# Optimization experiments

Hardware: AMD Instinct MI355X
Metric: run time of the kernel (lower is better)

## Reference

```python
import jax, jax.numpy as jnp
import numpy as np
from jax import lax

DEPTH = 2
HEADS = 8
TEMP = 1.0

def _ln_last(x, g, b, eps=1e-5):
    m = x.mean(-1, keepdims=True)
    v = ((x - m) ** 2).mean(-1, keepdims=True)
    return (x - m) / jnp.sqrt(v + eps) * g + b

def _ln_chan(x, g, b, eps=1e-6):
    # torch custom LayerNorm over channel dim of NCHW, biased var
    m = x.mean(1, keepdims=True)
    v = ((x - m) ** 2).mean(1, keepdims=True)
    return (x - m) / jnp.sqrt(v + eps) * g[None, :, None, None] + b[None, :, None, None]

def _conv3x3(x, w):
    return lax.conv_general_dilated(x, w, (1, 1), ((1, 1), (1, 1)),
                                    dimension_numbers=('NCHW', 'OIHW', 'NCHW'))

def _transformer(x, ln1_g, ln1_b, qkv_w, qkv_b, out_w, out_b, ln2_g, ln2_b,
                 mlp_w1, mlp_b1, mlp_w2, mlp_b2):
    dim = x.shape[-1]
    dh = dim // HEADS
    scale = dh ** -0.5
    for i in range(DEPTH):
        h = _ln_last(x, ln1_g[i], ln1_b[i])
        qkv = h @ qkv_w[i] + qkv_b[i]
        q, k, v = jnp.split(qkv, 3, axis=-1)
        sp = lambda t: t.reshape(t.shape[0], t.shape[1], HEADS, dh).transpose(0, 2, 1, 3)
        q, k, v = sp(q), sp(k), sp(v)
        attn = jax.nn.softmax(jnp.einsum('bhid,bhjd->bhij', q, k) * scale, axis=-1) / TEMP
        o = jnp.einsum('bhij,bhjd->bhid', attn, v).transpose(0, 2, 1, 3).reshape(x.shape)
        x = o @ out_w[i] + out_b[i] + x
        h = _ln_last(x, ln2_g[i], ln2_b[i])
        x = jax.nn.gelu(h @ mlp_w1[i] + mlp_b1[i], approximate=False) @ mlp_w2[i] + mlp_b2[i] + x
    return x

def _tacf(support_feature, query_feature, task_descriptor, ln1_g, ln1_b, qkv_w, qkv_b,
          out_w, out_b, ln2_g, ln2_b, mlp_w1, mlp_b1, mlp_w2, mlp_b2,
          rfm_ln_g, rfm_ln_b, rfm_conv1, rfm_conv2, rfm_conv3, rfm_conv4):
    n, c, h, w = support_feature.shape
    M = task_descriptor.shape[1]
    # descriptor generator: 'n c h w -> 1 (n h w) c', prepend descriptors
    sf = support_feature.transpose(0, 2, 3, 1).reshape(1, n * h * w, c)
    x = jnp.concatenate([task_descriptor, sf], axis=1)
    x = _transformer(x, ln1_g, ln1_b, qkv_w, qkv_b, out_w, out_b, ln2_g, ln2_b,
                     mlp_w1, mlp_b1, mlp_w2, mlp_b2)
    key0 = x[0, :M, :]  # (M, C)

    def region(feat):
        # mean over C of feat[:,None,c,h,w]*key[m,c] == matmul / C
        return jax.nn.sigmoid(jnp.einsum('bchw,mc->bmhw', feat, key0) / feat.shape[1])

    def map_fuse(reg, feat):
        # mean over m of (feat*task + feat) == feat*(mean_m(task)+1)
        return feat * (reg.mean(1, keepdims=True) + 1.0)

    def rfm(x4):
        t = _ln_chan(x4, rfm_ln_g, rfm_ln_b)
        t = jax.nn.relu(_conv3x3(t, rfm_conv1))
        t = jax.nn.relu(_conv3x3(t, rfm_conv2))
        t = jax.nn.relu(_conv3x3(t, rfm_conv3))
        t = _conv3x3(t, rfm_conv4)
        b_, T_, h_, w_ = t.shape
        t = jax.nn.sigmoid(t.reshape(b_, T_, h_ * w_))  # (B,T,HW)
        feat = x4.transpose(0, 2, 3, 1).reshape(b_, h_ * w_, -1)  # (B,HW,C)
        out = jnp.einsum('btp,bpc->btc', t, feat) / (h_ * w_)  # mean over HW
        return out.transpose(0, 2, 1)  # (B,C,T)

    qr = region(query_feature)
    sr = region(support_feature)
    aq = map_fuse(qr, query_feature)
    asp = map_fuse(sr, support_feature)
    return (rfm(asp), rfm(aq))

def setup_inputs() -> dict:
    key = jax.random.key(0)
    ks = jax.random.split(key, 12)
    B_S, B_Q, C, H, W = 25, 75, 128, 10, 10
    M, T, MLP = 16, 32, 512
    rn = lambda k, s, sc=1.0: jax.random.normal(k, s, dtype=jnp.float32) * sc
    return {
        'support_feature': rn(ks[0], (B_S, C, H, W)),
        'query_feature': rn(ks[1], (B_Q, C, H, W)),
        'task_descriptor': rn(ks[2], (1, M, C)),
        'ln1_g': jnp.ones((DEPTH, C), jnp.float32), 'ln1_b': jnp.zeros((DEPTH, C), jnp.float32),
        'qkv_w': rn(ks[3], (DEPTH, C, 3 * C), 0.02), 'qkv_b': jnp.zeros((DEPTH, 3 * C), jnp.float32),
        'out_w': rn(ks[4], (DEPTH, C, C), 0.02), 'out_b': jnp.zeros((DEPTH, C), jnp.float32),
        'ln2_g': jnp.ones((DEPTH, C), jnp.float32), 'ln2_b': jnp.zeros((DEPTH, C), jnp.float32),
        'mlp_w1': rn(ks[5], (DEPTH, C, MLP), 0.02), 'mlp_b1': jnp.zeros((DEPTH, MLP), jnp.float32),
        'mlp_w2': rn(ks[6], (DEPTH, MLP, C), 0.02), 'mlp_b2': jnp.zeros((DEPTH, C), jnp.float32),
        'rfm_ln_g': jnp.ones((C,), jnp.float32), 'rfm_ln_b': jnp.zeros((C,), jnp.float32),
        'rfm_conv1': rn(ks[7], (T, C, 3, 3), 0.05),
        'rfm_conv2': rn(ks[8], (T, T, 3, 3), 0.05),
        'rfm_conv3': rn(ks[9], (T, T, 3, 3), 0.05),
        'rfm_conv4': rn(ks[10], (T, T, 3, 3), 0.05),
    }

def reference(support_feature, query_feature, task_descriptor, ln1_g, ln1_b, qkv_w, qkv_b,
              out_w, out_b, ln2_g, ln2_b, mlp_w1, mlp_b1, mlp_w2, mlp_b2,
              rfm_ln_g, rfm_ln_b, rfm_conv1, rfm_conv2, rfm_conv3, rfm_conv4):
    return _tacf(support_feature, query_feature, task_descriptor, ln1_g, ln1_b, qkv_w, qkv_b,
                 out_w, out_b, ln2_g, ln2_b, mlp_w1, mlp_b1, mlp_w2, mlp_b2,
                 rfm_ln_g, rfm_ln_b, rfm_conv1, rfm_conv2, rfm_conv3, rfm_conv4)
```

## Files before the change

kernel.cpp:

```cpp
#include <hip/hip_runtime.h>
#include <math.h>

#define SEQ 2516
#define SEQP 2520
#define SEQP2 2560
#define CDIM 128

typedef __attribute__((ext_vector_type(8))) short short8;
typedef __attribute__((ext_vector_type(4))) float f32x4;

__device__ __forceinline__ float gelu_exact(float x) {
    return x * 0.5f * (1.0f + erff(x * 0.7071067811865475f));
}
__device__ __forceinline__ float fexp2(float x) { return __builtin_amdgcn_exp2f(x); }
__device__ __forceinline__ short f2bf(float f) {
    unsigned u = __float_as_uint(f);
    unsigned r = 0x7fffu + ((u >> 16) & 1u);
    return (short)((u + r) >> 16);
}
__device__ __forceinline__ short f2bf_trunc(float f) {
    return (short)(__float_as_uint(f) >> 16);
}

__global__ __launch_bounds__(64) void concat_ln_kernel(
// ... 71 lines not shown
    #pragma unroll
    for (int ns = 0; ns < 4; ++ns) {
        const int n = n0 + ns * 16 + c16;
        float bv = bias[n];
        #pragma unroll
        for (int r = 0; r < 4; ++r) {
            const int row = m0 + wave * 16 + quad * 4 + r;
            float v = acc[ns][r] + bv;
            if (region == 0)      Qbf[(size_t)row * 128 + n] = f2bf(v * SC);
            else if (region == 1) Kbf[(size_t)row * 128 + (n - 128)] = f2bf(v);
            else                  VTb[(size_t)(n - 256) * SEQP2 + row] = f2bf(v);
        }
    }
}

__global__ __launch_bounds__(256) void mlp_fused_kernel(
    const float* __restrict__ A, const float* __restrict__ W1,
    const float* __restrict__ b1, const float* __restrict__ W2,
    float* __restrict__ PARTG) {
    __shared__ __align__(16) short W1t[64 * 136];
    __shared__ __align__(16) short W2t[128 * 72];
    __shared__ __align__(16) short Ct[4 * 16 * 72];
    const int t = threadIdx.x;
    const int wave = t >> 6, lane = t & 63;
    const int quad = lane >> 4, c16 = lane & 15;
    const int m0 = blockIdx.x * 64;
    const int kz = blockIdx.y;
    const int n0 = kz * 64;
    #pragma unroll
    for (int pass = 0; pass < 4; ++pass) {
        int idx = t + pass * 256;
        int n = idx & 63, kc = idx >> 6;
        short8 wv;
        #pragma unroll
        for (int j = 0; j < 8; ++j)
            wv[j] = f2bf(W1[(size_t)(kc * 8 + j) * 512 + n0 + n]);
        *(short8*)&W1t[n * 136 + kc * 8] = wv;
    }
    {
        const int n = t & 127, half = t >> 7;
        #pragma unroll
        for (int c = 0; c < 4; ++c) {
            short8 wv;
            #pragma unroll
            for (int j = 0; j < 8; ++j)
                wv[j] = f2bf(W2[(size_t)(n0 + half * 32 + c * 8 + j) * 128 + n]);
            *(short8*)&W2t[n * 72 + half * 32 + c * 8] = wv;
        }
    }
    __syncthreads();
    const int am = m0 + wave * 16 + c16;
    f32x4 acc1[4];
    #pragma unroll
    for (int i = 0; i < 4; ++i) acc1[i] = (f32x4){0.f, 0.f, 0.f, 0.f};
    #pragma unroll
    for (int kk = 0; kk < 4; ++kk) {
        const float4* ap = (const float4*)(A + (size_t)am * 128 + kk * 32 + quad * 8);
        float4 a0 = ap[0], a1 = ap[1];
        short8 af;
        af[0] = f2bf(a0.x); af[1] = f2bf(a0.y); af[2] = f2bf(a0.z); af[3] = f2bf(a0.w);
        af[4] = f2bf(a1.x); af[5] = f2bf(a1.y); af[6] = f2bf(a1.z); af[7] = f2bf(a1.w);
        #pragma unroll
        for (int ns = 0; ns < 4; ++ns) {
            short8 wf = *(const short8*)&W1t[(ns * 16 + c16) * 136 + kk * 32 + quad * 8];
            acc1[ns] = __builtin_amdgcn_mfma_f32_16x16x32_bf16(af, wf, acc1[ns], 0, 0, 0);
        }
    }
    short* Cw = Ct + wave * 16 * 72;
    #pragma unroll
    for (int ns = 0; ns < 4; ++ns) {
        float bv = b1[n0 + ns * 16 + c16];
        #pragma unroll
        for (int r = 0; r < 4; ++r)
            Cw[(quad * 4 + r) * 72 + ns * 16 + c16] = f2bf(gelu_exact(acc1[ns][r] + bv));
    }
    f32x4 acc2[8];
    #pragma unroll
    for (int i = 0; i < 8; ++i) acc2[i] = (f32x4){0.f, 0.f, 0.f, 0.f};
    #pragma unroll
    for (int kk = 0; kk < 2; ++kk) {
        short8 af2 = *(const short8*)&Cw[c16 * 72 + kk * 32 + quad * 8];
        #pragma unroll
        for (int ns = 0; ns < 8; ++ns) {
            short8 wf = *(const short8*)&W2t[(ns * 16 + c16) * 72 + kk * 32 + quad * 8];
            acc2[ns] = __builtin_amdgcn_mfma_f32_16x16x32_bf16(af2, wf, acc2[ns], 0, 0, 0);
        }
    }
    float* dst = PARTG + (size_t)kz * SEQP2 * 128;
    #pragma unroll
    for (int ns = 0; ns < 8; ++ns) {
        #pragma unroll
        for (int r = 0; r < 4; ++r) {
            const int row = m0 + wave * 16 + quad * 4 + r;
            dst[(size_t)row * 128 + ns * 16 + c16] = acc2[ns][r];
        }
    }
}

__global__ __launch_bounds__(512) void combine_ln_kernel(
    const float* __restrict__ PARTG, const float* __restrict__ bias,
    const float* __restrict__ R, float* __restrict__ C, float* __restrict__ H,
    const float* __restrict__ g, const float* __restrict__ bb, int M) {
    __shared__ float ln[8][130];
    const int t = threadIdx.x;
    const int c = t & 127;
    const int grp = __builtin_amdgcn_readfirstlane(t >> 7);
    const int r0 = blockIdx.x * 8 + grp * 2;
    #pragma unroll
    for (int i = 0; i < 2; ++i) {
        const int row = r0 + i;
        float v = bias[c] + R[(size_t)row * 128 + c];
        #pragma unroll
        for (int kz = 0; kz < 8; ++kz)
            v += PARTG[(size_t)kz * SEQP2 * 128 + (size_t)row * 128 + c];
        ln[grp * 2 + i][c] = v;
        if (row < M) C[(size_t)row * 128 + c] = v;
    }
    __syncthreads();
    const int wv = t >> 6, l = t & 63;
    float x0 = ln[wv][l], x1 = ln[wv][l + 64];
    float s = x0 + x1;
    for (int off = 32; off > 0; off >>= 1) s += __shfl_down(s, off);
    float mean = __shfl(s, 0) * (1.f / 128.f);
    float d0 = x0 - mean, d1 = x1 - mean;
    float vv = d0 * d0 + d1 * d1;
    for (int off = 32; off > 0; off >>= 1) vv += __shfl_down(vv, off);
    float var = __shfl(vv, 0) * (1.f / 128.f);
    float rstd = rsqrtf(var + 1e-5f);
    const int hrow = blockIdx.x * 8 + wv;
    H[(size_t)hrow * 128 + l]      = d0 * rstd * g[l] + bb[l];
    H[(size_t)hrow * 128 + 64 + l] = d1 * rstd * g[l + 64] + bb[l + 64];
}

__global__ __launch_bounds__(512) void proj_merge_ln_kernel(
    const float* __restrict__ PART, const float* __restrict__ W,
    const float* __restrict__ bias, const float* __restrict__ R,
    float* __restrict__ C, float* __restrict__ H,
    const float* __restrict__ g, const float* __restrict__ bb, int M) {
    __shared__ float ln[8][130];
    const int t = threadIdx.x;
    const int c = t & 127;
    const int grp = __builtin_amdgcn_readfirstlane(t >> 7);
    const int r0 = blockIdx.x * 8 + grp * 2;
    float acc0 = 0.f, acc1 = 0.f;
    #pragma unroll
    for (int h = 0; h < 8; ++h) {
        const float* p0a = PART + ((size_t)h * SEQP + r0) * 20;
        const float* p1a = PART + ((size_t)(8 + h) * SEQP + r0) * 20;
        const float* p0b = p0a + 20;
        const float* p1b = p1a + 20;
        float m0 = p0a[16], l0 = p0a[17], m1 = p1a[16], l1 = p1a[17];
        float Ma = fmaxf(m0, m1);
        float w0 = fexp2(m0 - Ma), w1 = fexp2(m1 - Ma);
        float inva = 1.f / fmaf(l0, w0, l1 * w1);
        float c0a = w0 * inva, c1a = w1 * inva;
        m0 = p0b[16]; l0 = p0b[17]; m1 = p1b[16]; l1 = p1b[17];
        float Mb = fmaxf(m0, m1);
        w0 = fexp2(m0 - Mb); w1 = fexp2(m1 - Mb);
        float invb = 1.f / fmaf(l0, w0, l1 * w1);
        float c0b = w0 * invb, c1b = w1 * invb;
        #pragma unroll
        for (int kk = 0; kk < 4; ++kk) {
            const int k0 = h * 16 + kk * 4;
            float w_0 = W[(size_t)(k0 + 0) * 128 + c];
            float w_1 = W[(size_t)(k0 + 1) * 128 + c];
            float w_2 = W[(size_t)(k0 + 2) * 128 + c];
            float w_3 = W[(size_t)(k0 + 3) * 128 + c];
            float4 x0 = *(const float4*)&p0a[kk * 4];
            float4 y0 = *(const float4*)&p1a[kk * 4];
            float4 x1 = *(const float4*)&p0b[kk * 4];
            float4 y1 = *(const float4*)&p1b[kk * 4];
            float a00 = x0.x * c0a + y0.x * c1a;
            float a01 = x0.y * c0a + y0.y * c1a;
            float a02 = x0.z * c0a + y0.z * c1a;
            float a03 = x0.w * c0a + y0.w * c1a;
            float a10 = x1.x * c0b + y1.x * c1b;
            float a11 = x1.y * c0b + y1.y * c1b;
            float a12 = x1.z * c0b + y1.z * c1b;
            float a13 = x1.w * c0b + y1.w * c1b;
            acc0 = fmaf(a00, w_0, acc0); acc0 = fmaf(a01, w_1, acc0);
            acc0 = fmaf(a02, w_2, acc0); acc0 = fmaf(a03, w_3, acc0);
            acc1 = fmaf(a10, w_0, acc1); acc1 = fmaf(a11, w_1, acc1);
            acc1 = fmaf(a12, w_2, acc1); acc1 = fmaf(a13, w_3, acc1);
        }
    }
    float bv = bias[c];
    float v0 = acc0 + bv + R[(size_t)(r0 + 0) * 128 + c];
    float v1 = acc1 + bv + R[(size_t)(r0 + 1) * 128 + c];
    ln[grp * 2 + 0][c] = v0;
    ln[grp * 2 + 1][c] = v1;
    if (r0 + 0 < M) C[(size_t)(r0 + 0) * 128 + c] = v0;
    if (r0 + 1 < M) C[(size_t)(r0 + 1) * 128 + c] = v1;
    __syncthreads();
    const int wv = t >> 6, l = t & 63;
    float x0 = ln[wv][l], x1 = ln[wv][l + 64];
    float s = x0 + x1;
    for (int off = 32; off > 0; off >>= 1) s += __shfl_down(s, off);
    float mean = __shfl(s, 0) * (1.f / 128.f);
    float d0 = x0 - mean, d1 = x1 - mean;
    float vv = d0 * d0 + d1 * d1;
    for (int off = 32; off > 0; off >>= 1) vv += __shfl_down(vv, off);
    float var = __shfl(vv, 0) * (1.f / 128.f);
    float rstd = rsqrtf(var + 1e-5f);
    const int hrow = blockIdx.x * 8 + wv;
    H[(size_t)hrow * 128 + l]      = d0 * rstd * g[l] + bb[l];
    H[(size_t)hrow * 128 + 64 + l] = d1 * rstd * g[l + 64] + bb[l + 64];
}

__global__ __launch_bounds__(128) void attn_kernel(
    const short* __restrict__ Qbf, const short* __restrict__ Kbf,
    const short* __restrict__ VTb, float* __restrict__ PART) {
    __shared__ __align__(16) short sKs[9600];
    short* Ks = sKs;
    short* Vt = sKs + 3072;
    const int t = threadIdx.x;
    const int wave = t >> 6, lane = t & 63;
    const int quad = lane >> 4, c16 = lane & 15;
    short* Pw = sKs + 3072 + 2176 + wave * 16 * 136;
    const int head = blockIdx.y, z = blockIdx.z;
    const int qb = blockIdx.x * 32 + wave * 16;

    short8 qf;
    #pragma unroll
// ... 75 lines not shown
    for (int r = 0; r < 4; ++r) {
        float lr = l_[r];
        lr += __shfl_xor(lr, 1);
        lr += __shfl_xor(lr, 2);
        lr += __shfl_xor(lr, 4);
        lr += __shfl_xor(lr, 8);
        const int qrow = qb + quad * 4 + r;
        if (qrow < SEQ) {
            float* dst = PART + ((size_t)(z * 8 + head) * SEQP + qrow) * 20;
            dst[c16] = oacc[r];
            if (c16 == 0) { dst[16] = m_[r]; dst[17] = lr; }
        }
    }
}

__global__ __launch_bounds__(256) void region_fuse_stats_kernel(
    const float* __restrict__ sup, const float* __restrict__ qry,
    const float* __restrict__ X, float* __restrict__ fused,
    float* __restrict__ MEAN, float* __restrict__ RSTD) {
    __shared__ float key0[2048];
    __shared__ float rfac[100];
    const int b = blockIdx.x;
    const int t = threadIdx.x;
    const float* feat = (b < 25) ? (sup + (size_t)b * 12800) : (qry + (size_t)(b - 25) * 12800);
    for (int i = t; i < 2048; i += 256) key0[i] = X[i];
    __syncthreads();
    if (t < 100) {
        float dots[16];
        #pragma unroll
        for (int mm = 0; mm < 16; ++mm) dots[mm] = 0.f;
        float s = 0.f, ss = 0.f;
        for (int c = 0; c < 128; ++c) {
            float f = feat[c * 100 + t];
            s += f; ss += f * f;
            #pragma unroll
            for (int mm = 0; mm < 16; ++mm) dots[mm] += f * key0[mm * 128 + c];
        }
        float mean16 = 0.f;
        #pragma unroll
        for (int mm = 0; mm < 16; ++mm) mean16 += 1.f / (1.f + expf(-dots[mm] * (1.f / 128.f)));
        float r = mean16 * (1.f / 16.f) + 1.f;
        rfac[t] = r;
        float mr = s * (1.f / 128.f);
        float vr = ss * (1.f / 128.f) - mr * mr;
        MEAN[b * 128 + t] = mr * r;
        RSTD[b * 128 + t] = rsqrtf(vr * r * r + 1e-6f);
    }
    __syncthreads();
    for (int i = t; i < 12800; i += 256)
        fused[(size_t)b * 12800 + i] = feat[i] * rfac[i % 100];
}

__global__ __launch_bounds__(256) void conv1_split_kernel(
    const float* __restrict__ in, const float* __restrict__ w,
    const float* __restrict__ MEAN, const float* __restrict__ RSTD,
    const float* __restrict__ g, const float* __restrict__ bb,
    float* __restrict__ PARTC) {
    __shared__ float sin_[32 * 144];
    const int b = blockIdx.x;
    const int base_to = blockIdx.y * 8;
    const int cb = blockIdx.z * 32;
    const int t = threadIdx.x;
    const int h = __builtin_amdgcn_readfirstlane(t >> 7);
    const int p = t & 127;
    const int py = p / 10, px = p - py * 10;
    const bool active = p < 100;
    float acc[4] = {0.f, 0.f, 0.f, 0.f};
    for (int i = t; i < 32 * 144; i += 256) {
        int c = i / 144, pos = i - c * 144;
        int y = pos / 12 - 1, x = pos % 12 - 1;
        float v = 0.f;
        if ((unsigned)y < 10u && (unsigned)x < 10u) {
            int pp = y * 10 + x;
            float raw = in[(size_t)b * 12800 + (cb + c) * 100 + pp];
            v = (raw - MEAN[b * 128 + pp]) * RSTD[b * 128 + pp] * g[cb + c] + bb[cb + c];
        }
        sin_[i] = v;
    }
    __syncthreads();
    if (active) {
        const float* wbase = w + ((size_t)(base_to + h * 4) * 128 + cb) * 9;
        for (int c = 0; c < 32; ++c) {
            const float* sp = &sin_[c * 144 + py * 12 + px];
            float pix[9];
            #pragma unroll
            for (int k = 0; k < 9; ++k) pix[k] = sp[(k / 3) * 12 + (k % 3)];
            #pragma unroll
            for (int j = 0; j < 4; ++j) {
                const float* wq = wbase + ((size_t)j * 128 + c) * 9;
                #pragma unroll
                for (int k = 0; k < 9; ++k) acc[j] = fmaf(pix[k], wq[k], acc[j]);
            }
        }
        #pragma unroll
        for (int j = 0; j < 4; ++j)
            PARTC[((size_t)blockIdx.z * 100 + b) * 3200 + (base_to + h * 4 + j) * 100 + p] = acc[j];
    }
}

template<bool RELU, bool COMBINE>
__global__ __launch_bounds__(256) void conv3x3_to4_kernel(
    const float* __restrict__ in, const float* __restrict__ w,
    float* __restrict__ out) {
    __shared__ float sin_[32 * 144];
    const int b = blockIdx.x;
    const int base_to = blockIdx.y * 4;
    const int t = threadIdx.x;
    const int h = __builtin_amdgcn_readfirstlane(t >> 7);
    const int p = t & 127;
    const int py = p / 10, px = p - py * 10;
    const bool active = p < 100;
    float acc[2] = {0.f, 0.f};
    for (int i = t; i < 32 * 144; i += 256) {
        int c = i / 144, pos = i - c * 144;
        int y = pos / 12 - 1, x = pos % 12 - 1;
        float v = 0.f;
        if ((unsigned)y < 10u && (unsigned)x < 10u) {
            if (COMBINE) {
                const size_t base = (size_t)b * 3200 + c * 100 + y * 10 + x;
                v = in[base] + in[base + 320000] + in[base + 640000] + in[base + 960000];
                v = fmaxf(v, 0.f);
            } else {
                v = in[(size_t)b * 3200 + c * 100 + y * 10 + x];
            }
        }
        sin_[i] = v;
    }
    __syncthreads();
    if (active) {
        const float* wbase = w + ((size_t)(base_to + h * 2) * 32) * 9;
        for (int c = 0; c < 32; ++c) {
            const float* sp = &sin_[c * 144 + py * 12 + px];
            float pix[9];
            #pragma unroll
            for (int k = 0; k < 9; ++k) pix[k] = sp[(k / 3) * 12 + (k % 3)];
            #pragma unroll
            for (int j = 0; j < 2; ++j) {
                const float* wq = wbase + ((size_t)j * 32 + c) * 9;
                #pragma unroll
                for (int k = 0; k < 9; ++k) acc[j] = fmaf(pix[k], wq[k], acc[j]);
            }
        }
        #pragma unroll
        for (int j = 0; j < 2; ++j) {
            float v = acc[j];
            if (RELU) v = fmaxf(v, 0.f);
            out[(size_t)b * 3200 + (base_to + h * 2 + j) * 100 + p] = v;
        }
    }
}

__global__ __launch_bounds__(256) void conv4_rfm_kernel(
    const float* __restrict__ in, const float* __restrict__ w,
    const float* __restrict__ fused, float* __restrict__ out) {
    __shared__ float sin_[32 * 144];
    __shared__ float sig[4][104];
    const int b = blockIdx.x;
    const int base_to = blockIdx.y * 4;
    const int t = threadIdx.x;
    const int h = __builtin_amdgcn_readfirstlane(t >> 7);
    const int p = t & 127;
    const int py = p / 10, px = p - py * 10;
    const bool active = p < 100;
    float acc[2] = {0.f, 0.f};
    for (int i = t; i < 32 * 144; i += 256) {
        int c = i / 144, pos = i - c * 144;
        int y = pos / 12 - 1, x = pos % 12 - 1;
        float v = 0.f;
        if ((unsigned)y < 10u && (unsigned)x < 10u)
            v = in[(size_t)b * 3200 + c * 100 + y * 10 + x];
        sin_[i] = v;
    }
    __syncthreads();
    if (active) {
        const float* wbase = w + ((size_t)(base_to + h * 2) * 32) * 9;
        for (int c = 0; c < 32; ++c) {
            const float* sp = &sin_[c * 144 + py * 12 + px];
            float pix[9];
            #pragma unroll
            for (int k = 0; k < 9; ++k) pix[k] = sp[(k / 3) * 12 + (k % 3)];
            #pragma unroll
            for (int j = 0; j < 2; ++j) {
                const float* wq = wbase + ((size_t)j * 32 + c) * 9;
                #pragma unroll
                for (int k = 0; k < 9; ++k) acc[j] = fmaf(pix[k], wq[k], acc[j]);
            }
        }
        sig[h * 2 + 0][p] = 1.f / (1.f + expf(-acc[0]));
        sig[h * 2 + 1][p] = 1.f / (1.f + expf(-acc[1]));
    }
    __syncthreads();
    #pragma unroll
    for (int rep = 0; rep < 2; ++rep) {
        const int o = t + rep * 256;
        const int cc = o >> 2, ttl = o & 3;
        const float* fp = fused + (size_t)b * 12800 + cc * 100;
        float s = 0.f;
        for (int pp = 0; pp < 100; pp += 4) {
            float4 f4 = *(const float4*)&fp[pp];
            s += sig[ttl][pp] * f4.x + sig[ttl][pp + 1] * f4.y
               + sig[ttl][pp + 2] * f4.z + sig[ttl][pp + 3] * f4.w;
        }
        out[(size_t)b * 4096 + cc * 32 + base_to + ttl] = s * 0.01f;
    }
}

extern "C" void kernel_launch(void* const* d_in, const int* in_sizes, int n_in,
                              void* d_out, int out_size, void* d_ws, size_t ws_size,
                              hipStream_t stream) {
    (void)in_sizes; (void)n_in; (void)out_size; (void)ws_size;
    const float* sup    = (const float*)d_in[0];
    const float* qry    = (const float*)d_in[1];
    const float* td     = (const float*)d_in[2];
    const float* ln1_g  = (const float*)d_in[3];
    const float* ln1_b  = (const float*)d_in[4];
    const float* qkv_w  = (const float*)d_in[5];
    const float* qkv_b  = (const float*)d_in[6];
    const float* out_w  = (const float*)d_in[7];
// ... 3 lines not shown
    const float* mlp_w1 = (const float*)d_in[11];
    const float* mlp_b1 = (const float*)d_in[12];
    const float* mlp_w2 = (const float*)d_in[13];
    const float* mlp_b2 = (const float*)d_in[14];
    const float* rg     = (const float*)d_in[15];
    const float* rb     = (const float*)d_in[16];
    const float* c1     = (const float*)d_in[17];
    const float* c2     = (const float*)d_in[18];
    const float* c3     = (const float*)d_in[19];
    const float* c4     = (const float*)d_in[20];
    float* out = (float*)d_out;

    float* ws   = (float*)d_ws;
    float* X    = ws;
    float* H    = X + 327680;
    float* PARTC= H + 327680;
    float* FUSED= PARTC + 1280000;
    float* MEAN = FUSED + 1280000;
    float* RSTD = MEAN + 12800;
    float* CB1  = RSTD + 12800;
    float* CB2  = CB1 + 320000;
    short* Qbf  = (short*)(CB2 + 320000);
    short* Kbf  = Qbf + 327680;
    short* VTb  = Kbf + 327680;
    float* PARTG= (float*)(VTb + 327680);
    float* PART = PARTG;

    const int SG = (SEQ + 7) / 8;
    const int MT = (SEQ + 63) / 64;

    concat_ln_kernel<<<SEQ, 64, 0, stream>>>(td, sup, ln1_g, ln1_b, X, H);
    for (int i = 0; i < 2; ++i) {
        const int qmt    = (i == 0) ? MT : 1;
        const int atiles = (i == 0) ? (SEQ + 31) / 32 : 1;
        const int sg     = (i == 0) ? SG : 2;
        const int mmt    = (i == 0) ? MT : 1;
        qkv_mfma_kernel<<<dim3(MT, 6), 256, 0, stream>>>(
            H, qkv_w + (size_t)i * 128 * 384, qkv_b + i * 384, Qbf, Kbf, VTb, qmt);
        attn_kernel<<<dim3(atiles, 8, 2), 128, 0, stream>>>(Qbf, Kbf, VTb, PART);
        proj_merge_ln_kernel<<<sg, 512, 0, stream>>>(
            PART, out_w + (size_t)i * 128 * 128, out_b + i * 128, X, X, H,
            ln2_g + i * 128, ln2_b + i * 128, SEQ);
        mlp_fused_kernel<<<dim3(mmt, 8), 256, 0, stream>>>(
            H, mlp_w1 + (size_t)i * 128 * 512, mlp_b1 + i * 512,
            mlp_w2 + (size_t)i * 512 * 128, PARTG);
        const float* ng = (i == 0) ? ln1_g + 128 : ln1_g;
        const float* nb = (i == 0) ? ln1_b + 128 : ln1_b;
        combine_ln_kernel<<<sg, 512, 0, stream>>>(
            PARTG, mlp_b2 + i * 128, X, X, H, ng, nb, SEQ);
    }
    region_fuse_stats_kernel<<<100, 256, 0, stream>>>(sup, qry, X, FUSED, MEAN, RSTD);
    conv1_split_kernel<<<dim3(100, 4, 4), 256, 0, stream>>>(FUSED, c1, MEAN, RSTD, rg, rb, PARTC);
    conv3x3_to4_kernel<true,  true ><<<dim3(100, 8), 256, 0, stream>>>(PARTC, c2, CB2);
    conv3x3_to4_kernel<true,  false><<<dim3(100, 8), 256, 0, stream>>>(CB2, c3, CB1);
    conv4_rfm_kernel<<<dim3(100, 8), 256, 0, stream>>>(CB1, c4, FUSED, out);
}
```

Baseline: 316.6 us.

## Fuse out-projection, LN, MLP into one kernel and collapse conv chain into megakernel

The attention merge, output projection, residual, LayerNorm, both MLP GEMMs, a second residual and the next LayerNorm now run in one MFMA kernel per 64-row tile. This removes the split-K MLP partial buffer and two extra launches per layer. The region-fuse, channel LayerNorm and four 3x3 conv stages also merge into a single 512-thread kernel per image that keeps intermediates in shared memory. In exchange, parallelism drops: 40 blocks for the MLP instead of 320, and 100 blocks for the whole conv chain instead of up to 1600. Each block also loops serially over eight MLP weight chunks.

New measurement: 500.0 us. +57.9%, slower.

```diff
diff --git a/kernel.cpp b/kernel.cpp
--- a/kernel.cpp
+++ b/kernel.cpp
@@ -109,199 +109,6 @@
     }
 }
 
-__global__ __launch_bounds__(256) void mlp_fused_kernel(
-    const float* __restrict__ A, const float* __restrict__ W1,
-    const float* __restrict__ b1, const float* __restrict__ W2,
-    float* __restrict__ PARTG) {
-    __shared__ __align__(16) short W1t[64 * 136];
-    __shared__ __align__(16) short W2t[128 * 72];
-    __shared__ __align__(16) short Ct[4 * 16 * 72];
-    const int t = threadIdx.x;
-    const int wave = t >> 6, lane = t & 63;
-    const int quad = lane >> 4, c16 = lane & 15;
-    const int m0 = blockIdx.x * 64;
-    const int kz = blockIdx.y;
-    const int n0 = kz * 64;
-    #pragma unroll
-    for (int pass = 0; pass < 4; ++pass) {
-        int idx = t + pass * 256;
-        int n = idx & 63, kc = idx >> 6;
-        short8 wv;
-        #pragma unroll
-        for (int j = 0; j < 8; ++j)
-            wv[j] = f2bf(W1[(size_t)(kc * 8 + j) * 512 + n0 + n]);
-        *(short8*)&W1t[n * 136 + kc * 8] = wv;
-    }
-    {
-        const int n = t & 127, half = t >> 7;
-        #pragma unroll
-        for (int c = 0; c < 4; ++c) {
-            short8 wv;
-            #pragma unroll
-            for (int j = 0; j < 8; ++j)
-                wv[j] = f2bf(W2[(size_t)(n0 + half * 32 + c * 8 + j) * 128 + n]);
-            *(short8*)&W2t[n * 72 + half * 32 + c * 8] = wv;
-        }
-    }
-    __syncthreads();
-    const int am = m0 + wave * 16 + c16;
-    f32x4 acc1[4];
-    #pragma unroll
-    for (int i = 0; i < 4; ++i) acc1[i] = (f32x4){0.f, 0.f, 0.f, 0.f};
-    #pragma unroll
-    for (int kk = 0; kk < 4; ++kk) {
-        const float4* ap = (const float4*)(A + (size_t)am * 128 + kk * 32 + quad * 8);
-        float4 a0 = ap[0], a1 = ap[1];
-        short8 af;
-        af[0] = f2bf(a0.x); af[1] = f2bf(a0.y); af[2] = f2bf(a0.z); af[3] = f2bf(a0.w);
-        af[4] = f2bf(a1.x); af[5] = f2bf(a1.y); af[6] = f2bf(a1.z); af[7] = f2bf(a1.w);
-        #pragma unroll
-        for (int ns = 0; ns < 4; ++ns) {
-            short8 wf = *(const short8*)&W1t[(ns * 16 + c16) * 136 + kk * 32 + quad * 8];
-            acc1[ns] = __builtin_amdgcn_mfma_f32_16x16x32_bf16(af, wf, acc1[ns], 0, 0, 0);
-        }
-    }
-    short* Cw = Ct + wave * 16 * 72;
-    #pragma unroll
-    for (int ns = 0; ns < 4; ++ns) {
-        float bv = b1[n0 + ns * 16 + c16];
-        #pragma unroll
-        for (int r = 0; r < 4; ++r)
-            Cw[(quad * 4 + r) * 72 + ns * 16 + c16] = f2bf(gelu_exact(acc1[ns][r] + bv));
-    }
-    f32x4 acc2[8];
-    #pragma unroll
-    for (int i = 0; i < 8; ++i) acc2[i] = (f32x4){0.f, 0.f, 0.f, 0.f};
-    #pragma unroll
-    for (int kk = 0; kk < 2; ++kk) {
-        short8 af2 = *(const short8*)&Cw[c16 * 72 + kk * 32 + quad * 8];
-        #pragma unroll
-        for (int ns = 0; ns < 8; ++ns) {
-            short8 wf = *(const short8*)&W2t[(ns * 16 + c16) * 72 + kk * 32 + quad * 8];
-            acc2[ns] = __builtin_amdgcn_mfma_f32_16x16x32_bf16(af2, wf, acc2[ns], 0, 0, 0);
-        }
-    }
-    float* dst = PARTG + (size_t)kz * SEQP2 * 128;
-    #pragma unroll
-    for (int ns = 0; ns < 8; ++ns) {
-        #pragma unroll
-        for (int r = 0; r < 4; ++r) {
-            const int row = m0 + wave * 16 + quad * 4 + r;
-            dst[(size_t)row * 128 + ns * 16 + c16] = acc2[ns][r];
-        }
-    }
-}
-
-__global__ __launch_bounds__(512) void combine_ln_kernel(
-    const float* __restrict__ PARTG, const float* __restrict__ bias,
-    const float* __restrict__ R, float* __restrict__ C, float* __restrict__ H,
-    const float* __restrict__ g, const float* __restrict__ bb, int M) {
-    __shared__ float ln[8][130];
-    const int t = threadIdx.x;
-    const int c = t & 127;
-    const int grp = __builtin_amdgcn_readfirstlane(t >> 7);
-    const int r0 = blockIdx.x * 8 + grp * 2;
-    #pragma unroll
-    for (int i = 0; i < 2; ++i) {
-        const int row = r0 + i;
-        float v = bias[c] + R[(size_t)row * 128 + c];
-        #pragma unroll
-        for (int kz = 0; kz < 8; ++kz)
-            v += PARTG[(size_t)kz * SEQP2 * 128 + (size_t)row * 128 + c];
-        ln[grp * 2 + i][c] = v;
-        if (row < M) C[(size_t)row * 128 + c] = v;
-    }
-    __syncthreads();
-    const int wv = t >> 6, l = t & 63;
-    float x0 = ln[wv][l], x1 = ln[wv][l + 64];
-    float s = x0 + x1;
-    for (int off = 32; off > 0; off >>= 1) s += __shfl_down(s, off);
-    float mean = __shfl(s, 0) * (1.f / 128.f);
-    float d0 = x0 - mean, d1 = x1 - mean;
-    float vv = d0 * d0 + d1 * d1;
-    for (int off = 32; off > 0; off >>= 1) vv += __shfl_down(vv, off);
-    float var = __shfl(vv, 0) * (1.f / 128.f);
-    float rstd = rsqrtf(var + 1e-5f);
-    const int hrow = blockIdx.x * 8 + wv;
-    H[(size_t)hrow * 128 + l]      = d0 * rstd * g[l] + bb[l];
-    H[(size_t)hrow * 128 + 64 + l] = d1 * rstd * g[l + 64] + bb[l + 64];
-}
-
-__global__ __launch_bounds__(512) void proj_merge_ln_kernel(
-    const float* __restrict__ PART, const float* __restrict__ W,
-    const float* __restrict__ bias, const float* __restrict__ R,
-    float* __restrict__ C, float* __restrict__ H,
-    const float* __restrict__ g, const float* __restrict__ bb, int M) {
-    __shared__ float ln[8][130];
-    const int t = threadIdx.x;
-    const int c = t & 127;
-    const int grp = __builtin_amdgcn_readfirstlane(t >> 7);
-    const int r0 = blockIdx.x * 8 + grp * 2;
-    float acc0 = 0.f, acc1 = 0.f;
-    #pragma unroll
-    for (int h = 0; h < 8; ++h) {
-        const float* p0a = PART + ((size_t)h * SEQP + r0) * 20;
-        const float* p1a = PART + ((size_t)(8 + h) * SEQP + r0) * 20;
-        const float* p0b = p0a + 20;
-        const float* p1b = p1a + 20;
-        float m0 = p0a[16], l0 = p0a[17], m1 = p1a[16], l1 = p1a[17];
-        float Ma = fmaxf(m0, m1);
-        float w0 = fexp2(m0 - Ma), w1 = fexp2(m1 - Ma);
-        float inva = 1.f / fmaf(l0, w0, l1 * w1);
-        float c0a = w0 * inva, c1a = w1 * inva;
-        m0 = p0b[16]; l0 = p0b[17]; m1 = p1b[16]; l1 = p1b[17];
-        float Mb = fmaxf(m0, m1);
-        w0 = fexp2(m0 - Mb); w1 = fexp2(m1 - Mb);
-        float invb = 1.f / fmaf(l0, w0, l1 * w1);
-        float c0b = w0 * invb, c1b = w1 * invb;
-        #pragma unroll
-        for (int kk = 0; kk < 4; ++kk) {
-            const int k0 = h * 16 + kk * 4;
-            float w_0 = W[(size_t)(k0 + 0) * 128 + c];
-            float w_1 = W[(size_t)(k0 + 1) * 128 + c];
-            float w_2 = W[(size_t)(k0 + 2) * 128 + c];
-            float w_3 = W[(size_t)(k0 + 3) * 128 + c];
-            float4 x0 = *(const float4*)&p0a[kk * 4];
-            float4 y0 = *(const float4*)&p1a[kk * 4];
-            float4 x1 = *(const float4*)&p0b[kk * 4];
-            float4 y1 = *(const float4*)&p1b[kk * 4];
-            float a00 = x0.x * c0a + y0.x * c1a;
-            float a01 = x0.y * c0a + y0.y * c1a;
-            float a02 = x0.z * c0a + y0.z * c1a;
-            float a03 = x0.w * c0a + y0.w * c1a;
-            float a10 = x1.x * c0b + y1.x * c1b;
-            float a11 = x1.y * c0b + y1.y * c1b;
-            float a12 = x1.z * c0b + y1.z * c1b;
-            float a13 = x1.w * c0b + y1.w * c1b;
-            acc0 = fmaf(a00, w_0, acc0); acc0 = fmaf(a01, w_1, acc0);
-            acc0 = fmaf(a02, w_2, acc0); acc0 = fmaf(a03, w_3, acc0);
-            acc1 = fmaf(a10, w_0, acc1); acc1 = fmaf(a11, w_1, acc1);
-            acc1 = fmaf(a12, w_2, acc1); acc1 = fmaf(a13, w_3, acc1);
-        }
-    }
-    float bv = bias[c];
-    float v0 = acc0 + bv + R[(size_t)(r0 + 0) * 128 + c];
-    float v1 = acc1 + bv + R[(size_t)(r0 + 1) * 128 + c];
-    ln[grp * 2 + 0][c] = v0;
-    ln[grp * 2 + 1][c] = v1;
-    if (r0 + 0 < M) C[(size_t)(r0 + 0) * 128 + c] = v0;
-    if (r0 + 1 < M) C[(size_t)(r0 + 1) * 128 + c] = v1;
-    __syncthreads();
-    const int wv = t >> 6, l = t & 63;
-    float x0 = ln[wv][l], x1 = ln[wv][l + 64];
-    float s = x0 + x1;
-    for (int off = 32; off > 0; off >>= 1) s += __shfl_down(s, off);
-    float mean = __shfl(s, 0) * (1.f / 128.f);
-    float d0 = x0 - mean, d1 = x1 - mean;
-    float vv = d0 * d0 + d1 * d1;
-    for (int off = 32; off > 0; off >>= 1) vv += __shfl_down(vv, off);
-    float var = __shfl(vv, 0) * (1.f / 128.f);
-    float rstd = rsqrtf(var + 1e-5f);
-    const int hrow = blockIdx.x * 8 + wv;
-    H[(size_t)hrow * 128 + l]      = d0 * rstd * g[l] + bb[l];
-    H[(size_t)hrow * 128 + 64 + l] = d1 * rstd * g[l + 64] + bb[l + 64];
-}
-
 __global__ __launch_bounds__(128) void attn_kernel(
     const short* __restrict__ Qbf, const short* __restrict__ Kbf,
     const short* __restrict__ VTb, float* __restrict__ PART) {
@@ -407,194 +214,357 @@
     }
 }
 
-__global__ __launch_bounds__(256) void region_fuse_stats_kernel(
+__global__ __launch_bounds__(256) void pml_kernel(
+    const float* __restrict__ PART, const float* __restrict__ Wo,
+    const float* __restrict__ ob, const float* __restrict__ g2,
+    const float* __restrict__ bl2, const float* __restrict__ W1,
+    const float* __restrict__ b1, const float* __restrict__ W2,
+    const float* __restrict__ b2, const float* __restrict__ gn,
+    const float* __restrict__ bn,
+    float* __restrict__ X, float* __restrict__ H) {
+    __shared__ __align__(16) short hA[64 * 136];
+    __shared__ __align__(16) short U[23040];
+    const int t = threadIdx.x;
+    const int wave = t >> 6, lane = t & 63;
+    const int quad = lane >> 4, c16 = lane & 15;
+    const int m0 = blockIdx.x * 64;
+
+    for (int i = t; i < 16384; i += 256) {
+        int n = i & 127, k = i >> 7;
+        U[n * 136 + k] = f2bf(Wo[k * 128 + n]);
+    }
+    __syncthreads();
+    const int am = m0 + wave * 16 + c16;
+    const int amc = (am < SEQ) ? am : (SEQ - 1);
+    const bool okrow = (am < SEQ);
+    f32x4 acc[8];
+    #pragma unroll
+    for (int i = 0; i < 8; ++i) acc[i] = (f32x4){0.f, 0.f, 0.f, 0.f};
+    #pragma unroll
+    for (int kk = 0; kk < 4; ++kk) {
+        const int head = kk * 2 + (quad >> 1);
+        const int d0 = (quad & 1) * 8;
+        const float* P0 = PART + ((size_t)head * SEQP + amc) * 20;
+        const float* P1 = PART + ((size_t)(8 + head) * SEQP + amc) * 20;
+        float ma = P0[16], la = P0[17], mb = P1[16], lb = P1[17];
+        float Mx = fmaxf(ma, mb);
+        float w0 = fexp2(ma - Mx), w1 = fexp2(mb - Mx);
+        float inv = 1.f / fmaf(la, w0, lb * w1);
+        float c0 = okrow ? w0 * inv : 0.f;
+        float c1 = okrow ? w1 * inv : 0.f;
+        float4 xlo = *(const float4*)&P0[d0];
+        float4 xhi = *(const float4*)&P0[d0 + 4];
+        float4 ylo = *(const float4*)&P1[d0];
+        float4 yhi = *(const float4*)&P1[d0 + 4];
+        short8 af;
+        af[0] = f2bf(xlo.x * c0 + ylo.x * c1);
+        af[1] = f2bf(xlo.y * c0 + ylo.y * c1);
+        af[2] = f2bf(xlo.z * c0 + ylo.z * c1);
+        af[3] = f2bf(xlo.w * c0 + ylo.w * c1);
+        af[4] = f2bf(xhi.x * c0 + yhi.x * c1);
+        af[5] = f2bf(xhi.y * c0 + yhi.y * c1);
+        af[6] = f2bf(xhi.z * c0 + yhi.z * c1);
+        af[7] = f2bf(xhi.w * c0 + yhi.w * c1);
+        #pragma unroll
+        for (int ns = 0; ns < 8; ++ns) {
+            short8 wf = *(const short8*)&U[(ns * 16 + c16) * 136 + kk * 32 + quad * 8];
+            acc[ns] = __builtin_amdgcn_mfma_f32_16x16x32_bf16(af, wf, acc[ns], 0, 0, 0);
+        }
+    }
+    const int row0 = m0 + wave * 16 + quad * 4;
+    f32x4 xp[8];
+    #pragma unroll
+    for (int ns = 0; ns < 8; ++ns) {
+        const int col = ns * 16 + c16;
+        float bv = ob[col];
+        #pragma unroll
+        for (int r = 0; r < 4; ++r)
+            xp[ns][r] = acc[ns][r] + bv + X[(size_t)(row0 + r) * 128 + col];
+    }
+    #pragma unroll
+    for (int r = 0; r < 4; ++r) {
+        float sm = 0.f;
+        #pragma unroll
+        for (int ns = 0; ns < 8; ++ns) sm += xp[ns][r];
+        sm += __shfl_xor(sm, 1); sm += __shfl_xor(sm, 2);
+        sm += __shfl_xor(sm, 4); sm += __shfl_xor(sm, 8);
+        float mu = sm * (1.f / 128.f);
+        float vs = 0.f;
+        #pragma unroll
+        for (int ns = 0; ns < 8; ++ns) { float d = xp[ns][r] - mu; vs = fmaf(d, d, vs); }
+        vs += __shfl_xor(vs, 1); vs += __shfl_xor(vs, 2);
+        vs += __shfl_xor(vs, 4); vs += __shfl_xor(vs, 8);
+        float rs = rsqrtf(vs * (1.f / 128.f) + 1e-5f);
+        #pragma unroll
+        for (int ns = 0; ns < 8; ++ns) {
+            const int col = ns * 16 + c16;
+            float hv = (xp[ns][r] - mu) * rs * g2[col] + bl2[col];
+            hA[(wave * 16 + quad * 4 + r) * 136 + col] = f2bf(hv);
+        }
+    }
+
+    f32x4 acc2[8];
+    #pragma unroll
+    for (int i = 0; i < 8; ++i) acc2[i] = (f32x4){0.f, 0.f, 0.f, 0.f};
+    for (int kz = 0; kz < 8; ++kz) {
+        __syncthreads();
+        #pragma unroll
+        for (int pass = 0; pass < 4; ++pass) {
+            int idx = t + pass * 256;
+            int n = idx & 63, kc = idx >> 6;
+            short8 wv;
+            #pragma unroll
+            for (int j = 0; j < 8; ++j)
+                wv[j] = f2bf(W1[(size_t)(kc * 8 + j) * 512 + kz * 64 + n]);
+            *(short8*)&U[n * 136 + kc * 8] = wv;
+        }
+        {
+            const int n = t & 127, half = t >> 7;
+            #pragma unroll
+            for (int c = 0; c < 4; ++c) {
+                short8 wv;
+                #pragma unroll
+                for (int j = 0; j < 8; ++j)
+                    wv[j] = f2bf(W2[(size_t)(kz * 64 + half * 32 + c * 8 + j) * 128 + n]);
+                *(short8*)&U[8704 + n * 72 + half * 32 + c * 8] = wv;
+            }
+        }
+        __syncthreads();
+        f32x4 acc1[4];
+        #pragma unroll
+        for (int i = 0; i < 4; ++i) acc1[i] = (f32x4){0.f, 0.f, 0.f, 0.f};
+        #pragma unroll
+        for (int kk = 0; kk < 4; ++kk) {
+            short8 af = *(const short8*)&hA[(wave * 16 + c16) * 136 + kk * 32 + quad * 8];
+            #pragma unroll
+            for (int ns = 0; ns < 4; ++ns) {
+                short8 wf = *(const short8*)&U[(ns * 16 + c16) * 136 + kk * 32 + quad * 8];
+                acc1[ns] = __builtin_amdgcn_mfma_f32_16x16x32_bf16(af, wf, acc1[ns], 0, 0, 0);
+            }
+        }
+        short* Cw = &U[17920 + wave * 16 * 72];
+        #pragma unroll
+        for (int ns = 0; ns < 4; ++ns) {
+            float bv = b1[kz * 64 + ns * 16 + c16];
+            #pragma unroll
+            for (int r = 0; r < 4; ++r)
+                Cw[(quad * 4 + r) * 72 + ns * 16 + c16] = f2bf(gelu_exact(acc1[ns][r] + bv));
+        }
+        #pragma unroll
+        for (int kk = 0; kk < 2; ++kk) {
+            short8 af2 = *(const short8*)&Cw[c16 * 72 + kk * 32 + quad * 8];
+            #pragma unroll
+            for (int ns = 0; ns < 8; ++ns) {
+                short8 wf = *(const short8*)&U[8704 + (ns * 16 + c16) * 72 + kk * 32 + quad * 8];
+                acc2[ns] = __builtin_amdgcn_mfma_f32_16x16x32_bf16(af2, wf, acc2[ns], 0, 0, 0);
+            }
+        }
+    }
+    #pragma unroll
+    for (int ns = 0; ns < 8; ++ns) {
+        const int col = ns * 16 + c16;
+        float bv = b2[col];
+        #pragma unroll
+        for (int r = 0; r < 4; ++r) {
+            float v = acc2[ns][r] + bv + xp[ns][r];
+            xp[ns][r] = v;
+            X[(size_t)(row0 + r) * 128 + col] = v;
+        }
+    }
+    #pragma unroll
+    for (int r = 0; r < 4; ++r) {
+        float sm = 0.f;
+        #pragma unroll
+        for (int ns = 0; ns < 8; ++ns) sm += xp[ns][r];
+        sm += __shfl_xor(sm, 1); sm += __shfl_xor(sm, 2);
+        sm += __shfl_xor(sm, 4); sm += __shfl_xor(sm, 8);
+        float mu = sm * (1.f / 128.f);
+        float vs = 0.f;
+        #pragma unroll
+        for (int ns = 0; ns < 8; ++ns) { float d = xp[ns][r] - mu; vs = fmaf(d, d, vs); }
+        vs += __shfl_xor(vs, 1); vs += __shfl_xor(vs, 2);
+        vs += __shfl_xor(vs, 4); vs += __shfl_xor(vs, 8);
+        float rs = rsqrtf(vs * (1.f / 128.f) + 1e-5f);
+        #pragma unroll
+        for (int ns = 0; ns < 8; ++ns) {
+            const int col = ns * 16 + c16;
+            H[(size_t)(row0 + r) * 128 + col] = (xp[ns][r] - mu) * rs * gn[col] + bn[col];
+        }
+    }
+}
+
+__global__ __launch_bounds__(512) void conv_mega_kernel(
     const float* __restrict__ sup, const float* __restrict__ qry,
-    const float* __restrict__ X, float* __restrict__ fused,
-    float* __restrict__ MEAN, float* __restrict__ RSTD) {
-    __shared__ float key0[2048];
-    __shared__ float rfac[100];
+    const float* __restrict__ X,
+    const float* __restrict__ rg, const float* __restrict__ rb,
+    const float* __restrict__ w1, const float* __restrict__ w2,
+    const float* __restrict__ w3, const float* __restrict__ w4,
+    float* __restrict__ out) {
+    __shared__ float bufA[32 * 144];
+    __shared__ float bufB[32 * 144];
+    __shared__ float sigw[32][105];
+    __shared__ float dotsL[16][100];
+    __shared__ float rfacL[100], MEANL[100], RSTDL[100];
     const int b = blockIdx.x;
     const int t = threadIdx.x;
     const float* feat = (b < 25) ? (sup + (size_t)b * 12800) : (qry + (size_t)(b - 25) * 12800);
-    for (int i = t; i < 2048; i += 256) key0[i] = X[i];
+
+    for (int task = t; task < 1600; task += 512) {
+        int m = task / 100, p = task - m * 100;
+        const float* kp = X + m * 128;
+        float d = 0.f;
+        for (int c = 0; c < 128; ++c) d = fmaf(feat[c * 100 + p], kp[c], d);
+        dotsL[m][p] = d;
+    }
+    float s = 0.f, ss = 0.f;
+    if (t < 100) {
+        for (int c = 0; c < 128; ++c) {
+            float f = feat[c * 100 + t];
+            s += f; ss = fmaf(f, f, ss);
+        }
+    }
+    for (int i = t; i < 32 * 144; i += 512) bufB[i] = 0.f;
     __syncthreads();
     if (t < 100) {
-        float dots[16];
-        #pragma unroll
-        for (int mm = 0; mm < 16; ++mm) dots[mm] = 0.f;
-        float s = 0.f, ss = 0.f;
-        for (int c = 0; c < 128; ++c) {
-            float f = feat[c * 100 + t];
-            s += f; ss += f * f;
-            #pragma unroll
-            for (int mm = 0; mm < 16; ++mm) dots[mm] += f * key0[mm * 128 + c];
-        }
-        float mean16 = 0.f;
-        #pragma unroll
-        for (int mm = 0; mm < 16; ++mm) mean16 += 1.f / (1.f + expf(-dots[mm] * (1.f / 128.f)));
-        float r = mean16 * (1.f / 16.f) + 1.f;
-        rfac[t] = r;
+        float m16 = 0.f;
+        #pragma unroll
+        for (int mm = 0; mm < 16; ++mm)
+            m16 += 1.f / (1.f + expf(-dotsL[mm][t] * (1.f / 128.f)));
+        float r = m16 * (1.f / 16.f) + 1.f;
+        rfacL[t] = r;
         float mr = s * (1.f / 128.f);
         float vr = ss * (1.f / 128.f) - mr * mr;
-        MEAN[b * 128 + t] = mr * r;
-        RSTD[b * 128 + t] = rsqrtf(vr * r * r + 1e-6f);
+        MEANL[t] = mr * r;
+        RSTDL[t] = rsqrtf(vr * r * r + 1e-6f);
     }
     __syncthreads();
-    for (int i = t; i < 12800; i += 256)
-        fused[(size_t)b * 12800 + i] = feat[i] * rfac[i % 100];
-}
-
-__global__ __launch_bounds__(256) void conv1_split_kernel(
-    const float* __restrict__ in, const float* __restrict__ w,
-    const float* __restrict__ MEAN, const float* __restrict__ RSTD,
-    const float* __restrict__ g, const float* __restrict__ bb,
-    float* __restrict__ PARTC) {
-    __shared__ float sin_[32 * 144];
-    const int b = blockIdx.x;
-    const int base_to = blockIdx.y * 8;
-    const int cb = blockIdx.z * 32;
-    const int t = threadIdx.x;
-    const int h = __builtin_amdgcn_readfirstlane(t >> 7);
+
+    const int q = t >> 7;
     const int p = t & 127;
     const int py = p / 10, px = p - py * 10;
     const bool active = p < 100;
-    float acc[4] = {0.f, 0.f, 0.f, 0.f};
-    for (int i = t; i < 32 * 144; i += 256) {
-        int c = i / 144, pos = i - c * 144;
-        int y = pos / 12 - 1, x = pos % 12 - 1;
-        float v = 0.f;
-        if ((unsigned)y < 10u && (unsigned)x < 10u) {
-            int pp = y * 10 + x;
-            float raw = in[(size_t)b * 12800 + (cb + c) * 100 + pp];
-            v = (raw - MEAN[b * 128 + pp]) * RSTD[b * 128 + pp] * g[cb + c] + bb[cb + c];
-        }
-        sin_[i] = v;
+
+    float acc8[8] = {0.f, 0.f, 0.f, 0.f, 0.f, 0.f, 0.f, 0.f};
+    for (int cb = 0; cb < 128; cb += 32) {
+        for (int i = t; i < 32 * 144; i += 512) {
+            int c = i / 144, pos = i - c * 144;
+            int y = pos / 12 - 1, x = pos % 12 - 1;
+            float v = 0.f;
+            if ((unsigned)y < 10u && (unsigned)x < 10u) {
+                int pp = y * 10 + x;
+                v = (feat[(size_t)(cb + c) * 100 + pp] * rfacL[pp] - MEANL[pp])
+                    * RSTDL[pp] * rg[cb + c] + rb[cb + c];
+            }
+            bufA[i] = v;
+        }
+        __syncthreads();
+        if (active) {
+            const float* wbase = w1 + ((size_t)(q * 8) * 128 + cb) * 9;
+            for (int c = 0; c < 32; ++c) {
+                const float* sp = &bufA[c * 144 + py * 12 + px];
+                float pix[9];
+                #pragma unroll
+                for (int k = 0; k < 9; ++k) pix[k] = sp[(k / 3) * 12 + (k % 3)];
+                #pragma unroll
+                for (int j = 0; j < 8; ++j) {
+                    const float* wq = wbase + ((size_t)j * 128 + c) * 9;
+                    #pragma unroll
+                    for (int k = 0; k < 9; ++k) acc8[j] = fmaf(pix[k], wq[k], acc8[j]);
+                }
+            }
+        }
+        __syncthreads();
+    }
+    if (active) {
+        #pragma unroll
+        for (int j = 0; j < 8; ++j)
+            bufB[(q * 8 + j) * 144 + (py + 1) * 12 + (px + 1)] = fmaxf(acc8[j], 0.f);
     }
     __syncthreads();
-    if (active) {
-        const float* wbase = w + ((size_t)(base_to + h * 4) * 128 + cb) * 9;
-        for (int c = 0; c < 32; ++c) {
-            const float* sp = &sin_[c * 144 + py * 12 + px];
-            float pix[9];
-            #pragma unroll
-            for (int k = 0; k < 9; ++k) pix[k] = sp[(k / 3) * 12 + (k % 3)];
-            #pragma unroll
-            for (int j = 0; j < 4; ++j) {
-                const float* wq = wbase + ((size_t)j * 128 + c) * 9;
-                #pragma unroll
-                for (int k = 0; k < 9; ++k) acc[j] = fmaf(pix[k], wq[k], acc[j]);
-            }
-        }
-        #pragma unroll
-        for (int j = 0; j < 4; ++j)
-            PARTC[((size_t)blockIdx.z * 100 + b) * 3200 + (base_to + h * 4 + j) * 100 + p] = acc[j];
-    }
-}
-
-template<bool RELU, bool COMBINE>
-__global__ __launch_bounds__(256) void conv3x3_to4_kernel(
-    const float* __restrict__ in, const float* __restrict__ w,
-    float* __restrict__ out) {
-    __shared__ float sin_[32 * 144];
-    const int b = blockIdx.x;
-    const int base_to = blockIdx.y * 4;
-    const int t = threadIdx.x;
-    const int h = __builtin_amdgcn_readfirstlane(t >> 7);
-    const int p = t & 127;
-    const int py = p / 10, px = p - py * 10;
-    const bool active = p < 100;
-    float acc[2] = {0.f, 0.f};
-    for (int i = t; i < 32 * 144; i += 256) {
-        int c = i / 144, pos = i - c * 144;
-        int y = pos / 12 - 1, x = pos % 12 - 1;
-        float v = 0.f;
-        if ((unsigned)y < 10u && (unsigned)x < 10u) {
-            if (COMBINE) {
-                const size_t base = (size_t)b * 3200 + c * 100 + y * 10 + x;
-                v = in[base] + in[base + 320000] + in[base + 640000] + in[base + 960000];
-                v = fmaxf(v, 0.f);
-            } else {
-                v = in[(size_t)b * 3200 + c * 100 + y * 10 + x];
-            }
-        }
-        sin_[i] = v;
-    }
-    __syncthreads();
-    if (active) {
-        const float* wbase = w + ((size_t)(base_to + h * 2) * 32) * 9;
-        for (int c = 0; c < 32; ++c) {
-            const float* sp = &sin_[c * 144 + py * 12 + px];
-            float pix[9];
-            #pragma unroll
-            for (int k = 0; k < 9; ++k) pix[k] = sp[(k / 3) * 12 + (k % 3)];
-            #pragma unroll
-            for (int j = 0; j < 2; ++j) {
-                const float* wq = wbase + ((size_t)j * 32 + c) * 9;
-                #pragma unroll
-                for (int k = 0; k < 9; ++k) acc[j] = fmaf(pix[k], wq[k], acc[j]);
-            }
-        }
-        #pragma unroll
-        for (int j = 0; j < 2; ++j) {
-            float v = acc[j];
-            if (RELU) v = fmaxf(v, 0.f);
-            out[(size_t)b * 3200 + (base_to + h * 2 + j) * 100 + p] = v;
-        }
-    }
-}
-
-__global__ __launch_bounds__(256) void conv4_rfm_kernel(
-    const float* __restrict__ in, const float* __restrict__ w,
-    const float* __restrict__ fused, float* __restrict__ out) {
-    __shared__ float sin_[32 * 144];
-    __shared__ float sig[4][104];
-    const int b = blockIdx.x;
-    const int base_to = blockIdx.y * 4;
-    const int t = threadIdx.x;
-    const int h = __builtin_amdgcn_readfirstlane(t >> 7);
-    const int p = t & 127;
-    const int py = p / 10, px = p - py * 10;
-    const bool active = p < 100;
-    float acc[2] = {0.f, 0.f};
-    for (int i = t; i < 32 * 144; i += 256) {
-        int c = i / 144, pos = i - c * 144;
-        int y = pos / 12 - 1, x = pos % 12 - 1;
-        float v = 0.f;
-        if ((unsigned)y < 10u && (unsigned)x < 10u)
-            v = in[(size_t)b * 3200 + c * 100 + y * 10 + x];
-        sin_[i] = v;
-    }
-    __syncthreads();
-    if (active) {
-        const float* wbase = w + ((size_t)(base_to + h * 2) * 32) * 9;
-        for (int c = 0; c < 32; ++c) {
-            const float* sp = &sin_[c * 144 + py * 12 + px];
-            float pix[9];
-            #pragma unroll
-            for (int k = 0; k < 9; ++k) pix[k] = sp[(k / 3) * 12 + (k % 3)];
-            #pragma unroll
-            for (int j = 0; j < 2; ++j) {
-                const float* wq = wbase + ((size_t)j * 32 + c) * 9;
-                #pragma unroll
-                for (int k = 0; k < 9; ++k) acc[j] = fmaf(pix[k], wq[k], acc[j]);
-            }
-        }
-        sig[h * 2 + 0][p] = 1.f / (1.f + expf(-acc[0]));
-        sig[h * 2 + 1][p] = 1.f / (1.f + expf(-acc[1]));
-    }
-    __syncthreads();
-    #pragma unroll
-    for (int rep = 0; rep < 2; ++rep) {
-        const int o = t + rep * 256;
-        const int cc = o >> 2, ttl = o & 3;
-        const float* fp = fused + (size_t)b * 12800 + cc * 100;
-        float s = 0.f;
+
+    {
+        float a2[8] = {0.f, 0.f, 0.f, 0.f, 0.f, 0.f, 0.f, 0.f};
+        if (active) {
+            const float* wbase = w2 + (size_t)(q * 8) * 32 * 9;
+            for (int c = 0; c < 32; ++c) {
+                const float* sp = &bufB[c * 144 + py * 12 + px];
+                float pix[9];
+                #pragma unroll
+                for (int k = 0; k < 9; ++k) pix[k] = sp[(k / 3) * 12 + (k % 3)];
+                #pragma unroll
+                for (int j = 0; j < 8; ++j) {
+                    const float* wq = wbase + ((size_t)j * 32 + c) * 9;
+                    #pragma unroll
+                    for (int k = 0; k < 9; ++k) a2[j] = fmaf(pix[k], wq[k], a2[j]);
+                }
+            }
+        }
+        __syncthreads();
+        if (active) {
+            #pragma unroll
+            for (int j = 0; j < 8; ++j)
+                bufA[(q * 8 + j) * 144 + (py + 1) * 12 + (px + 1)] = fmaxf(a2[j], 0.f);
+        }
+        __syncthreads();
+    }
+    {
+        float a3[8] = {0.f, 0.f, 0.f, 0.f, 0.f, 0.f, 0.f, 0.f};
+        if (active) {
+            const float* wbase = w3 + (size_t)(q * 8) * 32 * 9;
+            for (int c = 0; c < 32; ++c) {
+                const float* sp = &bufA[c * 144 + py * 12 + px];
+                float pix[9];
+                #pragma unroll
+                for (int k = 0; k < 9; ++k) pix[k] = sp[(k / 3) * 12 + (k % 3)];
+                #pragma unroll
+                for (int j = 0; j < 8; ++j) {
+                    const float* wq = wbase + ((size_t)j * 32 + c) * 9;
+                    #pragma unroll
+                    for (int k = 0; k < 9; ++k) a3[j] = fmaf(pix[k], wq[k], a3[j]);
+                }
+            }
+        }
+        __syncthreads();
+        if (active) {
+            #pragma unroll
+            for (int j = 0; j < 8; ++j)
+                bufB[(q * 8 + j) * 144 + (py + 1) * 12 + (px + 1)] = fmaxf(a3[j], 0.f);
+        }
+        __syncthreads();
+    }
+    {
+        float a4[8] = {0.f, 0.f, 0.f, 0.f, 0.f, 0.f, 0.f, 0.f};
+        if (active) {
+            const float* wbase = w4 + (size_t)(q * 8) * 32 * 9;
+            for (int c = 0; c < 32; ++c) {
+                const float* sp = &bufB[c * 144 + py * 12 + px];
+                float pix[9];
+                #pragma unroll
+                for (int k = 0; k < 9; ++k) pix[k] = sp[(k / 3) * 12 + (k % 3)];
+                #pragma unroll
+                for (int j = 0; j < 8; ++j) {
+                    const float* wq = wbase + ((size_t)j * 32 + c) * 9;
+                    #pragma unroll
+                    for (int k = 0; k < 9; ++k) a4[j] = fmaf(pix[k], wq[k], a4[j]);
+                }
+            }
+            float rf = rfacL[p];
+            #pragma unroll
+            for (int j = 0; j < 8; ++j)
+                sigw[q * 8 + j][p] = rf / (1.f + expf(-a4[j]));
+        }
+        __syncthreads();
+    }
+    for (int o = t; o < 4096; o += 512) {
+        int cc = o >> 5, tt = o & 31;
+        const float* fp = feat + (size_t)cc * 100;
+        float acc = 0.f;
         for (int pp = 0; pp < 100; pp += 4) {
             float4 f4 = *(const float4*)&fp[pp];
-            s += sig[ttl][pp] * f4.x + sig[ttl][pp + 1] * f4.y
-               + sig[ttl][pp + 2] * f4.z + sig[ttl][pp + 3] * f4.w;
-        }
-        out[(size_t)b * 4096 + cc * 32 + base_to + ttl] = s * 0.01f;
+            acc += sigw[tt][pp] * f4.x + sigw[tt][pp + 1] * f4.y
+                 + sigw[tt][pp + 2] * f4.z + sigw[tt][pp + 3] * f4.w;
+        }
+        out[(size_t)b * 4096 + cc * 32 + tt] = acc * 0.01f;
     }
 }
 
@@ -628,44 +598,29 @@
     float* ws   = (float*)d_ws;
     float* X    = ws;
     float* H    = X + 327680;
-    float* PARTC= H + 327680;
-    float* FUSED= PARTC + 1280000;
-    float* MEAN = FUSED + 1280000;
-    float* RSTD = MEAN + 12800;
-    float* CB1  = RSTD + 12800;
-    float* CB2  = CB1 + 320000;
-    short* Qbf  = (short*)(CB2 + 320000);
+    short* Qbf  = (short*)(H + 327680);
     short* Kbf  = Qbf + 327680;
     short* VTb  = Kbf + 327680;
-    float* PARTG= (float*)(VTb + 327680);
-    float* PART = PARTG;
-
-    const int SG = (SEQ + 7) / 8;
+    float* PART = (float*)(VTb + 327680);
+
     const int MT = (SEQ + 63) / 64;
 
     concat_ln_kernel<<<SEQ, 64, 0, stream>>>(td, sup, ln1_g, ln1_b, X, H);
     for (int i = 0; i < 2; ++i) {
         const int qmt    = (i == 0) ? MT : 1;
         const int atiles = (i == 0) ? (SEQ + 31) / 32 : 1;
-        const int sg     = (i == 0) ? SG : 2;
-        const int mmt    = (i == 0) ? MT : 1;
+        const int pmt    = (i == 0) ? MT : 1;
         qkv_mfma_kernel<<<dim3(MT, 6), 256, 0, stream>>>(
             H, qkv_w + (size_t)i * 128 * 384, qkv_b + i * 384, Qbf, Kbf, VTb, qmt);
         attn_kernel<<<dim3(atiles, 8, 2), 128, 0, stream>>>(Qbf, Kbf, VTb, PART);
-        proj_merge_ln_kernel<<<sg, 512, 0, stream>>>(
-            PART, out_w + (size_t)i * 128 * 128, out_b + i * 128, X, X, H,
-            ln2_g + i * 128, ln2_b + i * 128, SEQ);
-        mlp_fused_kernel<<<dim3(mmt, 8), 256, 0, stream>>>(
-            H, mlp_w1 + (size_t)i * 128 * 512, mlp_b1 + i * 512,
-            mlp_w2 + (size_t)i * 512 * 128, PARTG);
         const float* ng = (i == 0) ? ln1_g + 128 : ln1_g;
         const float* nb = (i == 0) ? ln1_b + 128 : ln1_b;
-        combine_ln_kernel<<<sg, 512, 0, stream>>>(
-            PARTG, mlp_b2 + i * 128, X, X, H, ng, nb, SEQ);
-    }
-    region_fuse_stats_kernel<<<100, 256, 0, stream>>>(sup, qry, X, FUSED, MEAN, RSTD);
-    conv1_split_kernel<<<dim3(100, 4, 4), 256, 0, stream>>>(FUSED, c1, MEAN, RSTD, rg, rb, PARTC);
-    conv3x3_to4_kernel<true,  true ><<<dim3(100, 8), 256, 0, stream>>>(PARTC, c2, CB2);
-    conv3x3_to4_kernel<true,  false><<<dim3(100, 8), 256, 0, stream>>>(CB2, c3, CB1);
-    conv4_rfm_kernel<<<dim3(100, 8), 256, 0, stream>>>(CB1, c4, FUSED, out);
-}
+        pml_kernel<<<pmt, 256, 0, stream>>>(
+            PART, out_w + (size_t)i * 128 * 128, out_b + i * 128,
+            ln2_g + i * 128, ln2_b + i * 128,
+            mlp_w1 + (size_t)i * 128 * 512, mlp_b1 + i * 512,
+            mlp_w2 + (size_t)i * 512 * 128, mlp_b2 + i * 128,
+            ng, nb, X, H);
+    }
+    conv_mega_kernel<<<100, 512, 0, stream>>>(sup, qry, X, rg, rb, c1, c2, c3, c4, out);
+}
```
